# Optimization experiments

Measured on AMD Instinct MI355X. Metric: run time of the kernel, lower is better.

The kernel has to match this reference:

```python
import jax, jax.numpy as jnp
import numpy as np

EMBED_DIM = 1024
NUM_HEADS = 16
HEAD_DIM = EMBED_DIM // NUM_HEADS


def setup_inputs() -> dict:
    key = jax.random.key(0)
    kx, kw1, kb1, kw2, kb2 = jax.random.split(key, 5)
    D = EMBED_DIM
    # torch nn.Linear default init: U(-1/sqrt(in), 1/sqrt(in)); use scaled uniform
    lim = 1.0 / np.sqrt(D)
    return {
        "x": jax.random.normal(kx, (2, 2048, D), dtype=jnp.float32),
        "w_qkv": jax.random.uniform(kw1, (D, 3 * D), jnp.float32, -lim, lim),
        "b_qkv": jax.random.uniform(kb1, (3 * D,), jnp.float32, -lim, lim),
        "w_o": jax.random.uniform(kw2, (D, D), jnp.float32, -lim, lim),
        "b_o": jax.random.uniform(kb2, (D,), jnp.float32, -lim, lim),
    }


def reference(x, w_qkv, b_qkv, w_o, b_o):
    B, S, D = x.shape
    H, hd = NUM_HEADS, HEAD_DIM
    qkv = x @ w_qkv + b_qkv                       # [B,S,3D]
    qkv = qkv.reshape(B, S, H, 3, hd)             # per-head [q|k|v] blocks of size hd
    q = qkv[:, :, :, 0].transpose(0, 2, 1, 3)     # [B,H,S,hd]
    k = qkv[:, :, :, 1].transpose(0, 2, 1, 3)
    v = qkv[:, :, :, 2].transpose(0, 2, 1, 3)
    scale = hd ** -0.5
    scores = jnp.einsum('bhqd,bhkd->bhqk', q, k) * scale
    attn = jax.nn.softmax(scores, axis=-1)
    out = jnp.einsum('bhqk,bhkd->bhqd', attn, v)  # [B,H,S,hd]
    out = out.transpose(0, 2, 1, 3).reshape(B, S, D)
    return out @ w_o + b_o
```

## Files before the change

kernel.cpp:

```cpp
#include <hip/hip_runtime.h>

typedef __attribute__((ext_vector_type(8))) _Float16 half8;
typedef __attribute__((ext_vector_type(4))) _Float16 half4;
typedef __attribute__((ext_vector_type(4))) float f32x4;
typedef __attribute__((ext_vector_type(16))) float f32x16;
typedef __attribute__((ext_vector_type(4))) int i32x4;

typedef __attribute__((address_space(1))) void* gptr_t;
typedef __attribute__((address_space(3))) void* lptr_t;
#define GLL16(g, l) __builtin_amdgcn_global_load_lds((gptr_t)(g), (lptr_t)(l), 16, 0, 0)

__device__ __forceinline__ float fast_exp2(float x) {
  float r;
  asm volatile("v_exp_f32 %0, %1" : "=v"(r) : "v"(x));
  return r;
}


__global__ void prep_kernel(const float* __restrict__ x, _Float16* __restrict__ xh,
                            const float* __restrict__ w_qkv, _Float16* __restrict__ wqkvT,
                            const float* __restrict__ w_o, _Float16* __restrict__ woT) {
  __shared__ _Float16 lds[64][72];
  const int bid = blockIdx.x;
  const int t = threadIdx.x;
  if (bid < 4096) {
    size_t i = (size_t)bid * 256 + t;
    float4 v = *reinterpret_cast<const float4*>(x + i * 4);
    half4 o = { (_Float16)v.x, (_Float16)v.y, (_Float16)v.z, (_Float16)v.w };
    *reinterpret_cast<half4*>(xh + i * 4) = o;
    return;
  }
  const float* w; _Float16* wt; int N, bx, by;
  if (bid < 4096 + 768) { int b = bid - 4096; w = w_qkv; wt = wqkvT; N = 3072; bx = b % 48; by = b / 48; }
  else                  { int b = bid - 4864; w = w_o;   wt = woT;   N = 1024; bx = b & 15; by = b >> 4; }
  const int n0 = bx * 64, k0 = by * 64;
#pragma unroll
  for (int rep = 0; rep < 4; ++rep) {
    int k = rep * 16 + (t >> 4);
    int nc = (t & 15) * 4;
    float4 v = *reinterpret_cast<const float4*>(&w[(size_t)(k0 + k) * N + n0 + nc]);
    lds[nc + 0][k] = (_Float16)v.x;
    lds[nc + 1][k] = (_Float16)v.y;
    lds[nc + 2][k] = (_Float16)v.z;
    lds[nc + 3][k] = (_Float16)v.w;
  }
  __syncthreads();
#pragma unroll
  for (int rep = 0; rep < 2; ++rep) {
    int ch = rep * 256 + t;
    int n = ch >> 3, kc = ch & 7;
    half8 o = *reinterpret_cast<const half8*>(&lds[n][kc * 8]);
    *reinterpret_cast<half8*>(&wt[(size_t)(n0 + n) * 1024 + k0 + kc * 8]) = o;
  }
}


__global__ __launch_bounds__(256, 2)
void gemm_qkv(const _Float16* __restrict__ A, const _Float16* __restrict__ Bt,
              const float* __restrict__ bias,
              _Float16* __restrict__ qh, _Float16* __restrict__ kh,
              _Float16* __restrict__ vT) {
  __shared__ __align__(16) _Float16 Ah[128 * 64];
  __shared__ __align__(16) _Float16 Bh[128 * 64];
  const int t = threadIdx.x;
  const int w = t >> 6, ln = t & 63, G = ln >> 4, c = ln & 15;
  const int m0 = blockIdx.y * 128, n0 = blockIdx.x * 128;
  const int wr = w >> 1, wc = w & 1;
  f32x4 acc[4][4] = {};
  for (int kt = 0; kt < 1024; kt += 64) {
#pragma unroll
    for (int i = 0; i < 4; ++i) {
      int ch = i * 256 + t;
      int row = ch >> 3, kc = ch & 7;
      int kk = kt + ((kc ^ (row & 7)) << 3);
      int ldsbase = (i * 256 + w * 64) * 8;
      GLL16(A + (size_t)(m0 + row) * 1024 + kk, Ah + ldsbase);
      GLL16(Bt + (size_t)(n0 + row) * 1024 + kk, Bh + ldsbase);
    }
    __syncthreads();
    half8 aF[2][4], bF[2][4];
#pragma unroll
    for (int ks = 0; ks < 2; ++ks)
#pragma unroll
      for (int i = 0; i < 4; ++i) {
        int ra = wr * 64 + i * 16 + c;
        aF[ks][i] = *reinterpret_cast<const half8*>(&Ah[ra * 64 + (((ks * 4 + G) ^ (ra & 7)) << 3)]);
        int rb = wc * 64 + i * 16 + c;
        bF[ks][i] = *reinterpret_cast<const half8*>(&Bh[rb * 64 + (((ks * 4 + G) ^ (rb & 7)) << 3)]);
      }
#pragma unroll
    for (int ks = 0; ks < 2; ++ks)
#pragma unroll
      for (int mi = 0; mi < 4; ++mi)
#pragma unroll
        for (int ni = 0; ni < 4; ++ni)
          acc[mi][ni] = __builtin_amdgcn_mfma_f32_16x16x32_f16(aF[ks][mi], bF[ks][ni], acc[mi][ni], 0, 0, 0);
    __syncthreads();
  }
  const int mbase = m0 + wr * 64, nbase = n0 + wc * 64;
  const int Gp = ((G & 1) << 1) | (G >> 1);
#pragma unroll
  for (int ni = 0; ni < 4; ++ni) {
    int n = nbase + ni * 16 + c;
    float bv = bias[n];
    int h = n / 192;
    int rem = n - h * 192;
    int tt = rem >> 6, d = rem & 63;
#pragma unroll
    for (int mi = 0; mi < 4; ++mi) {
      if (tt == 2) {
        int mb = mbase + mi * 16;
        int bb = mb >> 11, s0 = mb & 2047;
        size_t bh = (size_t)(bb * 16 + h);
        half4 o = { (_Float16)(acc[mi][ni][0] + bv), (_Float16)(acc[mi][ni][1] + bv),
                    (_Float16)(acc[mi][ni][2] + bv), (_Float16)(acc[mi][ni][3] + bv) };
        *reinterpret_cast<half4*>(&vT[(bh * 64 + d) * 2048 + s0 + 4 * Gp]) = o;
      } else {
#pragma unroll
        for (int r = 0; r < 4; ++r) {
          int m = mbase + mi * 16 + 4 * G + r;
          int bb = m >> 11, s = m & 2047;
          float val = acc[mi][ni][r] + bv;
          size_t bh = (size_t)(bb * 16 + h);
          if (tt == 0) qh[(bh * 2048 + s) * 64 + d] = (_Float16)(val * (0.125f * 1.44269504089f));
          else         kh[(bh * 2048 + s) * 64 + d] = (_Float16)val;
        }
      }
    }
  }
}


__global__ __launch_bounds__(256, 2)
void gemm_o(const _Float16* __restrict__ A, const _Float16* __restrict__ Bt,
            const float* __restrict__ bias, float* __restrict__ outf) {
  __shared__ __align__(16) _Float16 Ah[128 * 64];
  __shared__ __align__(16) _Float16 Bh[64 * 64];
  const int t = threadIdx.x;
  const int w = t >> 6, ln = t & 63, G = ln >> 4, c = ln & 15;
  const int m0 = blockIdx.y * 128, n0 = blockIdx.x * 64;
  const int wr = w >> 1, wc = w & 1;
  f32x4 acc[4][2] = {};
  for (int kt = 0; kt < 1024; kt += 64) {
#pragma unroll
    for (int i = 0; i < 4; ++i) {
      int ch = i * 256 + t;
      int row = ch >> 3, kc = ch & 7;
      int kk = kt + ((kc ^ (row & 7)) << 3);
      GLL16(A + (size_t)(m0 + row) * 1024 + kk, Ah + (i * 256 + w * 64) * 8);
    }
#pragma unroll
    for (int i = 0; i < 2; ++i) {
      int ch = i * 256 + t;
      int row = ch >> 3, kc = ch & 7;
      int kk = kt + ((kc ^ (row & 7)) << 3);
      GLL16(Bt + (size_t)(n0 + row) * 1024 + kk, Bh + (i * 256 + w * 64) * 8);
    }
    __syncthreads();
    half8 aF[2][4], bF[2][2];
#pragma unroll
    for (int ks = 0; ks < 2; ++ks) {
#pragma unroll
      for (int i = 0; i < 4; ++i) {
        int ra = wr * 64 + i * 16 + c;
        aF[ks][i] = *reinterpret_cast<const half8*>(&Ah[ra * 64 + (((ks * 4 + G) ^ (ra & 7)) << 3)]);
      }
#pragma unroll
      for (int i = 0; i < 2; ++i) {
        int rb = wc * 32 + i * 16 + c;
        bF[ks][i] = *reinterpret_cast<const half8*>(&Bh[rb * 64 + (((ks * 4 + G) ^ (rb & 7)) << 3)]);
      }
    }
#pragma unroll
    for (int ks = 0; ks < 2; ++ks)
#pragma unroll
      for (int mi = 0; mi < 4; ++mi)
#pragma unroll
        for (int ni = 0; ni < 2; ++ni)
          acc[mi][ni] = __builtin_amdgcn_mfma_f32_16x16x32_f16(aF[ks][mi], bF[ks][ni], acc[mi][ni], 0, 0, 0);
    __syncthreads();
  }
  const int mbase = m0 + wr * 64, nbase = n0 + wc * 32;
#pragma unroll
  for (int ni = 0; ni < 2; ++ni) {
    int n = nbase + ni * 16 + c;
    float bv = bias[n];
#pragma unroll
    for (int mi = 0; mi < 4; ++mi)
#pragma unroll
      for (int r = 0; r < 4; ++r) {
        int m = mbase + mi * 16 + 4 * G + r;
        outf[(size_t)m * 1024 + n] = acc[mi][ni][r] + bv;
      }
  }
}


__global__ __launch_bounds__(256, 1)
void attn_kernel(const _Float16* __restrict__ qh, const _Float16* __restrict__ kh,
                 const _Float16* __restrict__ vT, _Float16* __restrict__ ao) {
  __shared__ __align__(16) _Float16 Kt[3][64 * 64];
  __shared__ __align__(16) _Float16 Vt[4][64 * 64];
  const int t = threadIdx.x;
  const int w = t >> 6, ln = t & 63, lo = ln & 31, hi = ln >> 5;
  const int bid = blockIdx.x;
  const int xcd = bid & 7, tt = bid >> 3;
  const int bh = xcd * 4 + (tt >> 4);
  const int qb = tt & 15;
  const int q0 = qb * 128 + w * 32;
  const _Float16* qp = qh + (size_t)bh * 2048 * 64;
  const _Float16* kp = kh + (size_t)bh * 2048 * 64;
  const _Float16* vp = vT + (size_t)bh * 64 * 2048;

  half8 qf[4];
#pragma unroll
  for (int sl = 0; sl < 4; ++sl)
    qf[sl] = *reinterpret_cast<const half8*>(qp + (size_t)(q0 + lo) * 64 + sl * 16 + hi * 8);

  f32x16 O0 = {}, O1 = {};
  f32x16 S0, S1;
  float plsum = 0.f;
  unsigned pk[4][4];

  auto stage = [&](int kb, int vb, int jt) {
#pragma unroll
    for (int i = 0; i < 2; ++i) {
      int ch = i * 256 + t;
      int row = ch >> 3, cc = ch & 7;
      int sw = ((cc ^ ((row ^ (row >> 3)) & 7)) << 3);
      int ldsbase = (i * 256 + w * 64) * 8;
      GLL16(kp + (size_t)(jt + row) * 64 + sw, &Kt[kb][ldsbase]);
      GLL16(vp + (size_t)row * 2048 + jt + sw, &Vt[vb][ldsbase]);
    }
  };

  auto qkt = [&](int kb) {
    f32x16 a = {}, b = {};
#pragma unroll
    for (int sl = 0; sl < 4; ++sl) {
      const int ch = sl * 2 + hi;
      const int r0 = lo, r1 = 32 + lo;
      half8 k0 = *reinterpret_cast<const half8*>(&Kt[kb][r0 * 64 + ((ch ^ ((r0 ^ (r0 >> 3)) & 7)) << 3)]);
      a = __builtin_amdgcn_mfma_f32_32x32x16_f16(k0, qf[sl], a, 0, 0, 0);
      half8 k1 = *reinterpret_cast<const half8*>(&Kt[kb][r1 * 64 + ((ch ^ ((r1 ^ (r1 >> 3)) & 7)) << 3)]);
      b = __builtin_amdgcn_mfma_f32_32x32x16_f16(k1, qf[sl], b, 0, 0, 0);
    }
    S0 = a; S1 = b;
  };

  auto pv = [&](int vb) {
#pragma unroll
    for (int kb2 = 0; kb2 < 4; ++kb2) {
      i32x4 pi = { (int)pk[kb2][0], (int)pk[kb2][1], (int)pk[kb2][2], (int)pk[kb2][3] };
      half8 pf = __builtin_bit_cast(half8, pi);
      const int ch = kb2 * 2 + hi;
      const int r0 = lo, r1 = 32 + lo;
      half8 v0 = *reinterpret_cast<const half8*>(&Vt[vb][r0 * 64 + ((ch ^ ((r0 ^ (r0 >> 3)) & 7)) << 3)]);
      O0 = __builtin_amdgcn_mfma_f32_32x32x16_f16(v0, pf, O0, 0, 0, 0);
      half8 v1 = *reinterpret_cast<const half8*>(&Vt[vb][r1 * 64 + ((ch ^ ((r1 ^ (r1 >> 3)) & 7)) << 3)]);
      O1 = __builtin_amdgcn_mfma_f32_32x32x16_f16(v1, pf, O1, 0, 0, 0);
    }
  };

  auto smpack = [&]() {
    float e0[16], e1[16];
#pragma unroll
    for (int i = 0; i < 16; ++i) e0[i] = fast_exp2(S0[i]);
#pragma unroll
    for (int i = 0; i < 16; ++i) e1[i] = fast_exp2(S1[i]);
    float sm[8];
#pragma unroll
    for (int i = 0; i < 8; ++i) sm[i] = (e0[i] + e0[i + 8]) + (e1[i] + e1[i + 8]);
#pragma unroll
    for (int i = 0; i < 4; ++i) sm[i] += sm[i + 4];
    plsum += (sm[0] + sm[1]) + (sm[2] + sm[3]);
#pragma unroll
    for (int kh2 = 0; kh2 < 2; ++kh2)
#pragma unroll
      for (int j = 0; j < 4; ++j) {
        pk[kh2][j]     = __builtin_bit_cast(unsigned, __builtin_amdgcn_cvt_pkrtz(e0[kh2 * 8 + 2 * j], e0[kh2 * 8 + 2 * j + 1]));
        pk[2 + kh2][j] = __builtin_bit_cast(unsigned, __builtin_amdgcn_cvt_pkrtz(e1[kh2 * 8 + 2 * j], e1[kh2 * 8 + 2 * j + 1]));
      }
  };

  stage(0, 0, 0);
  stage(1, 1, 64);
  stage(2, 2, 128);
  asm volatile("s_waitcnt vmcnt(8)" ::: "memory");
  __builtin_amdgcn_s_barrier();
  qkt(0);
  asm volatile("s_waitcnt vmcnt(4)" ::: "memory");
  __builtin_amdgcn_s_barrier();

  for (int it = 0; it < 31; ++it) {
    if (it < 29) {
      int T = it + 3;
      stage(T % 3, T & 3, T * 64);
    }
    smpack();
    __builtin_amdgcn_s_setprio(1);
    qkt((it + 1) % 3);
    pv(it & 3);
    __builtin_amdgcn_s_setprio(0);
    if (it < 29) asm volatile("s_waitcnt vmcnt(4)" ::: "memory");
    else         asm volatile("s_waitcnt vmcnt(0)" ::: "memory");
    __builtin_amdgcn_s_barrier();
  }
  smpack();
  pv(31 & 3);

  float lsum = plsum + __shfl_xor(plsum, 32);
  float inv = 1.f / lsum;
  const int bb = bh >> 4, hd_i = bh & 15;
  const size_t srow = (size_t)bb * 2048 + q0 + lo;
  _Float16* aob = ao + srow * 1024 + hd_i * 64 + hi * 4;
#pragma unroll
  for (int rq = 0; rq < 4; ++rq) {
    half4 o0 = { (_Float16)(O0[4 * rq] * inv), (_Float16)(O0[4 * rq + 1] * inv),
                 (_Float16)(O0[4 * rq + 2] * inv), (_Float16)(O0[4 * rq + 3] * inv) };
    *reinterpret_cast<half4*>(aob + rq * 8) = o0;
    half4 o1 = { (_Float16)(O1[4 * rq] * inv), (_Float16)(O1[4 * rq + 1] * inv),
                 (_Float16)(O1[4 * rq + 2] * inv), (_Float16)(O1[4 * rq + 3] * inv) };
    *reinterpret_cast<half4*>(aob + 32 + rq * 8) = o1;
  }
}


extern "C" void kernel_launch(void* const* d_in, const int* in_sizes, int n_in,
                              void* d_out, int out_size, void* d_ws, size_t ws_size,
                              hipStream_t stream) {
  const float* x     = (const float*)d_in[0];
  const float* w_qkv = (const float*)d_in[1];
  const float* b_qkv = (const float*)d_in[2];
  const float* w_o   = (const float*)d_in[3];
  const float* b_o   = (const float*)d_in[4];
  float* out = (float*)d_out;
  char* ws = (char*)d_ws;
  _Float16* xh    = (_Float16*)(ws);
  _Float16* wqkvT = (_Float16*)(ws + ((size_t)8  << 20));
  _Float16* woT   = (_Float16*)(ws + ((size_t)14 << 20));
  _Float16* qh    = (_Float16*)(ws + ((size_t)16 << 20));
  _Float16* kh    = (_Float16*)(ws + ((size_t)24 << 20));
  _Float16* vT    = (_Float16*)(ws + ((size_t)32 << 20));
  _Float16* ao    = (_Float16*)(ws + ((size_t)40 << 20));

  prep_kernel<<<5120, 256, 0, stream>>>(x, xh, w_qkv, wqkvT, w_o, woT);
  gemm_qkv<<<dim3(24, 32), 256, 0, stream>>>(xh, wqkvT, b_qkv, qh, kh, vT);
  attn_kernel<<<512, 256, 0, stream>>>(qh, kh, vT, ao);
  gemm_o<<<dim3(16, 32), 256, 0, stream>>>(ao, woT, b_o, out);
}
```

Measured before the change: 114.2 us.

## Double-buffer LDS tiles in QKV and output GEMMs, replace modulo with counters

Both projection GEMMs now use two LDS buffers so the global-to-LDS load of the next K tile is issued before computing on the current one, overlapping memory latency with MFMA work. The attention loop replaces the `% 3` buffer index computations with rolling counters. Doubling LDS use (64KB for QKV) may reduce occupancy below the two blocks per CU requested by the launch bounds. A single barrier per iteration relies on the hardware waiting for outstanding loads before the barrier.

```diff
diff --git a/kernel.cpp b/kernel.cpp
--- a/kernel.cpp
+++ b/kernel.cpp
@@ -60,33 +60,40 @@
               const float* __restrict__ bias,
               _Float16* __restrict__ qh, _Float16* __restrict__ kh,
               _Float16* __restrict__ vT) {
-  __shared__ __align__(16) _Float16 Ah[128 * 64];
-  __shared__ __align__(16) _Float16 Bh[128 * 64];
+  __shared__ __align__(16) _Float16 Ah[2][128 * 64];
+  __shared__ __align__(16) _Float16 Bh[2][128 * 64];
   const int t = threadIdx.x;
   const int w = t >> 6, ln = t & 63, G = ln >> 4, c = ln & 15;
   const int m0 = blockIdx.y * 128, n0 = blockIdx.x * 128;
   const int wr = w >> 1, wc = w & 1;
   f32x4 acc[4][4] = {};
-  for (int kt = 0; kt < 1024; kt += 64) {
+
+  auto stage = [&](int b, int kt) {
 #pragma unroll
     for (int i = 0; i < 4; ++i) {
       int ch = i * 256 + t;
       int row = ch >> 3, kc = ch & 7;
       int kk = kt + ((kc ^ (row & 7)) << 3);
       int ldsbase = (i * 256 + w * 64) * 8;
-      GLL16(A + (size_t)(m0 + row) * 1024 + kk, Ah + ldsbase);
-      GLL16(Bt + (size_t)(n0 + row) * 1024 + kk, Bh + ldsbase);
-    }
-    __syncthreads();
+      GLL16(A + (size_t)(m0 + row) * 1024 + kk, &Ah[b][ldsbase]);
+      GLL16(Bt + (size_t)(n0 + row) * 1024 + kk, &Bh[b][ldsbase]);
+    }
+  };
+
+  stage(0, 0);
+  __syncthreads();
+  int buf = 0;
+  for (int kt = 0; kt < 1024; kt += 64) {
+    if (kt < 960) stage(buf ^ 1, kt + 64);
     half8 aF[2][4], bF[2][4];
 #pragma unroll
     for (int ks = 0; ks < 2; ++ks)
 #pragma unroll
       for (int i = 0; i < 4; ++i) {
         int ra = wr * 64 + i * 16 + c;
-        aF[ks][i] = *reinterpret_cast<const half8*>(&Ah[ra * 64 + (((ks * 4 + G) ^ (ra & 7)) << 3)]);
+        aF[ks][i] = *reinterpret_cast<const half8*>(&Ah[buf][ra * 64 + (((ks * 4 + G) ^ (ra & 7)) << 3)]);
         int rb = wc * 64 + i * 16 + c;
-        bF[ks][i] = *reinterpret_cast<const half8*>(&Bh[rb * 64 + (((ks * 4 + G) ^ (rb & 7)) << 3)]);
+        bF[ks][i] = *reinterpret_cast<const half8*>(&Bh[buf][rb * 64 + (((ks * 4 + G) ^ (rb & 7)) << 3)]);
       }
 #pragma unroll
     for (int ks = 0; ks < 2; ++ks)
@@ -96,6 +103,7 @@
         for (int ni = 0; ni < 4; ++ni)
           acc[mi][ni] = __builtin_amdgcn_mfma_f32_16x16x32_f16(aF[ks][mi], bF[ks][ni], acc[mi][ni], 0, 0, 0);
     __syncthreads();
+    buf ^= 1;
   }
   const int mbase = m0 + wr * 64, nbase = n0 + wc * 64;
   const int Gp = ((G & 1) << 1) | (G >> 1);
@@ -134,41 +142,48 @@
 __global__ __launch_bounds__(256, 2)
 void gemm_o(const _Float16* __restrict__ A, const _Float16* __restrict__ Bt,
             const float* __restrict__ bias, float* __restrict__ outf) {
-  __shared__ __align__(16) _Float16 Ah[128 * 64];
-  __shared__ __align__(16) _Float16 Bh[64 * 64];
+  __shared__ __align__(16) _Float16 Ah[2][128 * 64];
+  __shared__ __align__(16) _Float16 Bh[2][64 * 64];
   const int t = threadIdx.x;
   const int w = t >> 6, ln = t & 63, G = ln >> 4, c = ln & 15;
   const int m0 = blockIdx.y * 128, n0 = blockIdx.x * 64;
   const int wr = w >> 1, wc = w & 1;
   f32x4 acc[4][2] = {};
-  for (int kt = 0; kt < 1024; kt += 64) {
+
+  auto stage = [&](int b, int kt) {
 #pragma unroll
     for (int i = 0; i < 4; ++i) {
       int ch = i * 256 + t;
       int row = ch >> 3, kc = ch & 7;
       int kk = kt + ((kc ^ (row & 7)) << 3);
-      GLL16(A + (size_t)(m0 + row) * 1024 + kk, Ah + (i * 256 + w * 64) * 8);
+      GLL16(A + (size_t)(m0 + row) * 1024 + kk, &Ah[b][(i * 256 + w * 64) * 8]);
     }
 #pragma unroll
     for (int i = 0; i < 2; ++i) {
       int ch = i * 256 + t;
       int row = ch >> 3, kc = ch & 7;
       int kk = kt + ((kc ^ (row & 7)) << 3);
-      GLL16(Bt + (size_t)(n0 + row) * 1024 + kk, Bh + (i * 256 + w * 64) * 8);
-    }
-    __syncthreads();
+      GLL16(Bt + (size_t)(n0 + row) * 1024 + kk, &Bh[b][(i * 256 + w * 64) * 8]);
+    }
+  };
+
+  stage(0, 0);
+  __syncthreads();
+  int buf = 0;
+  for (int kt = 0; kt < 1024; kt += 64) {
+    if (kt < 960) stage(buf ^ 1, kt + 64);
     half8 aF[2][4], bF[2][2];
 #pragma unroll
     for (int ks = 0; ks < 2; ++ks) {
 #pragma unroll
       for (int i = 0; i < 4; ++i) {
         int ra = wr * 64 + i * 16 + c;
-        aF[ks][i] = *reinterpret_cast<const half8*>(&Ah[ra * 64 + (((ks * 4 + G) ^ (ra & 7)) << 3)]);
+        aF[ks][i] = *reinterpret_cast<const half8*>(&Ah[buf][ra * 64 + (((ks * 4 + G) ^ (ra & 7)) << 3)]);
       }
 #pragma unroll
       for (int i = 0; i < 2; ++i) {
         int rb = wc * 32 + i * 16 + c;
-        bF[ks][i] = *reinterpret_cast<const half8*>(&Bh[rb * 64 + (((ks * 4 + G) ^ (rb & 7)) << 3)]);
+        bF[ks][i] = *reinterpret_cast<const half8*>(&Bh[buf][rb * 64 + (((ks * 4 + G) ^ (rb & 7)) << 3)]);
       }
     }
 #pragma unroll
@@ -179,6 +194,7 @@
         for (int ni = 0; ni < 2; ++ni)
           acc[mi][ni] = __builtin_amdgcn_mfma_f32_16x16x32_f16(aF[ks][mi], bF[ks][ni], acc[mi][ni], 0, 0, 0);
     __syncthreads();
+    buf ^= 1;
   }
   const int mbase = m0 + wr * 64, nbase = n0 + wc * 32;
 #pragma unroll
@@ -292,19 +308,19 @@
   asm volatile("s_waitcnt vmcnt(4)" ::: "memory");
   __builtin_amdgcn_s_barrier();
 
+  int kb_w = 0, kb_n = 1;
   for (int it = 0; it < 31; ++it) {
-    if (it < 29) {
-      int T = it + 3;
-      stage(T % 3, T & 3, T * 64);
-    }
+    if (it < 29) stage(kb_w, (it + 3) & 3, (it + 3) * 64);
     smpack();
     __builtin_amdgcn_s_setprio(1);
-    qkt((it + 1) % 3);
+    qkt(kb_n);
     pv(it & 3);
     __builtin_amdgcn_s_setprio(0);
     if (it < 29) asm volatile("s_waitcnt vmcnt(4)" ::: "memory");
     else         asm volatile("s_waitcnt vmcnt(0)" ::: "memory");
     __builtin_amdgcn_s_barrier();
+    if (++kb_w == 3) kb_w = 0;
+    if (++kb_n == 3) kb_n = 0;
   }
   smpack();
   pv(31 & 3);
```

Result: no change. 116.0 us (+1.6%).

## Widen attention KV tile to 128 keys with double-buffered K and triple-buffered V

Applied to the files above, without the earlier changes.

The attention kernel now processes 128 keys per iteration instead of 64. K uses two LDS buffers and V three, with a 16-chunk XOR swizzle for the wider V rows. The main loop is unrolled by two and waits for all outstanding loads (vmcnt(0)) before each barrier. This halves the number of loop iterations and barriers, at the cost of more registers for S and P and a shallower prefetch pipeline, which could expose load latency.

```diff
diff --git a/kernel.cpp b/kernel.cpp
--- a/kernel.cpp
+++ b/kernel.cpp
@@ -199,8 +199,8 @@
 __global__ __launch_bounds__(256, 1)
 void attn_kernel(const _Float16* __restrict__ qh, const _Float16* __restrict__ kh,
                  const _Float16* __restrict__ vT, _Float16* __restrict__ ao) {
-  __shared__ __align__(16) _Float16 Kt[3][64 * 64];
-  __shared__ __align__(16) _Float16 Vt[4][64 * 64];
+  __shared__ __align__(16) _Float16 Kt[2][128 * 64];
+  __shared__ __align__(16) _Float16 Vt[3][64 * 128];
   const int t = threadIdx.x;
   const int w = t >> 6, ln = t & 63, lo = ln & 31, hi = ln >> 5;
   const int bid = blockIdx.x;
@@ -218,96 +218,118 @@
     qf[sl] = *reinterpret_cast<const half8*>(qp + (size_t)(q0 + lo) * 64 + sl * 16 + hi * 8);
 
   f32x16 O0 = {}, O1 = {};
-  f32x16 S0, S1;
+  f32x16 S0, S1, S2, S3;
   float plsum = 0.f;
-  unsigned pk[4][4];
-
-  auto stage = [&](int kb, int vb, int jt) {
-#pragma unroll
-    for (int i = 0; i < 2; ++i) {
+  unsigned pk[8][4];
+
+  auto stageK = [&](int kb, int jt) {
+#pragma unroll
+    for (int i = 0; i < 4; ++i) {
       int ch = i * 256 + t;
       int row = ch >> 3, cc = ch & 7;
-      int sw = ((cc ^ ((row ^ (row >> 3)) & 7)) << 3);
-      int ldsbase = (i * 256 + w * 64) * 8;
-      GLL16(kp + (size_t)(jt + row) * 64 + sw, &Kt[kb][ldsbase]);
-      GLL16(vp + (size_t)row * 2048 + jt + sw, &Vt[vb][ldsbase]);
+      int sw = (cc ^ ((row ^ (row >> 3)) & 7)) << 3;
+      GLL16(kp + (size_t)(jt + row) * 64 + sw, &Kt[kb][(i * 256 + w * 64) * 8]);
+    }
+  };
+  auto stageV = [&](int vb, int jt) {
+#pragma unroll
+    for (int i = 0; i < 4; ++i) {
+      int ch = i * 256 + t;
+      int row = ch >> 4, cc = ch & 15;
+      int sw = (cc ^ ((row ^ (row >> 4)) & 15)) << 3;
+      GLL16(vp + (size_t)row * 2048 + jt + sw, &Vt[vb][(i * 256 + w * 64) * 8]);
     }
   };
 
   auto qkt = [&](int kb) {
-    f32x16 a = {}, b = {};
+    f32x16 a0 = {}, a1 = {}, a2 = {}, a3 = {};
 #pragma unroll
     for (int sl = 0; sl < 4; ++sl) {
       const int ch = sl * 2 + hi;
-      const int r0 = lo, r1 = 32 + lo;
+      const int r0 = lo, r1 = 32 + lo, r2 = 64 + lo, r3 = 96 + lo;
       half8 k0 = *reinterpret_cast<const half8*>(&Kt[kb][r0 * 64 + ((ch ^ ((r0 ^ (r0 >> 3)) & 7)) << 3)]);
-      a = __builtin_amdgcn_mfma_f32_32x32x16_f16(k0, qf[sl], a, 0, 0, 0);
+      a0 = __builtin_amdgcn_mfma_f32_32x32x16_f16(k0, qf[sl], a0, 0, 0, 0);
       half8 k1 = *reinterpret_cast<const half8*>(&Kt[kb][r1 * 64 + ((ch ^ ((r1 ^ (r1 >> 3)) & 7)) << 3)]);
-      b = __builtin_amdgcn_mfma_f32_32x32x16_f16(k1, qf[sl], b, 0, 0, 0);
-    }
-    S0 = a; S1 = b;
+      a1 = __builtin_amdgcn_mfma_f32_32x32x16_f16(k1, qf[sl], a1, 0, 0, 0);
+      half8 k2 = *reinterpret_cast<const half8*>(&Kt[kb][r2 * 64 + ((ch ^ ((r2 ^ (r2 >> 3)) & 7)) << 3)]);
+      a2 = __builtin_amdgcn_mfma_f32_32x32x16_f16(k2, qf[sl], a2, 0, 0, 0);
+      half8 k3 = *reinterpret_cast<const half8*>(&Kt[kb][r3 * 64 + ((ch ^ ((r3 ^ (r3 >> 3)) & 7)) << 3)]);
+      a3 = __builtin_amdgcn_mfma_f32_32x32x16_f16(k3, qf[sl], a3, 0, 0, 0);
+    }
+    S0 = a0; S1 = a1; S2 = a2; S3 = a3;
   };
 
   auto pv = [&](int vb) {
 #pragma unroll
-    for (int kb2 = 0; kb2 < 4; ++kb2) {
+    for (int kb2 = 0; kb2 < 8; ++kb2) {
       i32x4 pi = { (int)pk[kb2][0], (int)pk[kb2][1], (int)pk[kb2][2], (int)pk[kb2][3] };
       half8 pf = __builtin_bit_cast(half8, pi);
       const int ch = kb2 * 2 + hi;
       const int r0 = lo, r1 = 32 + lo;
-      half8 v0 = *reinterpret_cast<const half8*>(&Vt[vb][r0 * 64 + ((ch ^ ((r0 ^ (r0 >> 3)) & 7)) << 3)]);
+      half8 v0 = *reinterpret_cast<const half8*>(&Vt[vb][r0 * 128 + ((ch ^ ((r0 ^ (r0 >> 4)) & 15)) << 3)]);
       O0 = __builtin_amdgcn_mfma_f32_32x32x16_f16(v0, pf, O0, 0, 0, 0);
-      half8 v1 = *reinterpret_cast<const half8*>(&Vt[vb][r1 * 64 + ((ch ^ ((r1 ^ (r1 >> 3)) & 7)) << 3)]);
+      half8 v1 = *reinterpret_cast<const half8*>(&Vt[vb][r1 * 128 + ((ch ^ ((r1 ^ (r1 >> 4)) & 15)) << 3)]);
       O1 = __builtin_amdgcn_mfma_f32_32x32x16_f16(v1, pf, O1, 0, 0, 0);
     }
   };
 
-  auto smpack = [&]() {
-    float e0[16], e1[16];
-#pragma unroll
-    for (int i = 0; i < 16; ++i) e0[i] = fast_exp2(S0[i]);
-#pragma unroll
-    for (int i = 0; i < 16; ++i) e1[i] = fast_exp2(S1[i]);
-    float sm[8];
-#pragma unroll
-    for (int i = 0; i < 8; ++i) sm[i] = (e0[i] + e0[i + 8]) + (e1[i] + e1[i + 8]);
-#pragma unroll
-    for (int i = 0; i < 4; ++i) sm[i] += sm[i + 4];
-    plsum += (sm[0] + sm[1]) + (sm[2] + sm[3]);
+  auto smp1 = [&](f32x16& S, int base) {
+    float e[16];
+#pragma unroll
+    for (int i = 0; i < 16; ++i) e[i] = fast_exp2(S[i]);
+    float s4[4];
+#pragma unroll
+    for (int i = 0; i < 4; ++i) s4[i] = (e[i] + e[i + 4]) + (e[i + 8] + e[i + 12]);
+    plsum += (s4[0] + s4[1]) + (s4[2] + s4[3]);
 #pragma unroll
     for (int kh2 = 0; kh2 < 2; ++kh2)
 #pragma unroll
-      for (int j = 0; j < 4; ++j) {
-        pk[kh2][j]     = __builtin_bit_cast(unsigned, __builtin_amdgcn_cvt_pkrtz(e0[kh2 * 8 + 2 * j], e0[kh2 * 8 + 2 * j + 1]));
-        pk[2 + kh2][j] = __builtin_bit_cast(unsigned, __builtin_amdgcn_cvt_pkrtz(e1[kh2 * 8 + 2 * j], e1[kh2 * 8 + 2 * j + 1]));
-      }
-  };
-
-  stage(0, 0, 0);
-  stage(1, 1, 64);
-  stage(2, 2, 128);
+      for (int j = 0; j < 4; ++j)
+        pk[base + kh2][j] = __builtin_bit_cast(unsigned,
+            __builtin_amdgcn_cvt_pkrtz(e[kh2 * 8 + 2 * j], e[kh2 * 8 + 2 * j + 1]));
+  };
+  auto smpack = [&]() { smp1(S0, 0); smp1(S1, 2); smp1(S2, 4); smp1(S3, 6); };
+
+  stageK(0, 0);   stageV(0, 0);
+  stageK(1, 128); stageV(1, 128);
   asm volatile("s_waitcnt vmcnt(8)" ::: "memory");
   __builtin_amdgcn_s_barrier();
   qkt(0);
-  asm volatile("s_waitcnt vmcnt(4)" ::: "memory");
+  asm volatile("s_waitcnt vmcnt(0)" ::: "memory");
   __builtin_amdgcn_s_barrier();
 
-  for (int it = 0; it < 31; ++it) {
-    if (it < 29) {
-      int T = it + 3;
-      stage(T % 3, T & 3, T * 64);
-    }
+  int vbr = 0, vbw = 2;
+  auto bump3 = [](int& v) { if (++v == 3) v = 0; };
+#pragma unroll 1
+  for (int it2 = 0; it2 < 7; ++it2) {
+    const int tE = 2 * it2;
+    stageK(0, (tE + 2) * 128); stageV(vbw, (tE + 2) * 128);
     smpack();
     __builtin_amdgcn_s_setprio(1);
-    qkt((it + 1) % 3);
-    pv(it & 3);
+    qkt(1);
+    pv(vbr);
     __builtin_amdgcn_s_setprio(0);
-    if (it < 29) asm volatile("s_waitcnt vmcnt(4)" ::: "memory");
-    else         asm volatile("s_waitcnt vmcnt(0)" ::: "memory");
+    asm volatile("s_waitcnt vmcnt(0)" ::: "memory");
     __builtin_amdgcn_s_barrier();
+    bump3(vbr); bump3(vbw);
+    stageK(1, (tE + 3) * 128); stageV(vbw, (tE + 3) * 128);
+    smpack();
+    __builtin_amdgcn_s_setprio(1);
+    qkt(0);
+    pv(vbr);
+    __builtin_amdgcn_s_setprio(0);
+    asm volatile("s_waitcnt vmcnt(0)" ::: "memory");
+    __builtin_amdgcn_s_barrier();
+    bump3(vbr); bump3(vbw);
   }
   smpack();
-  pv(31 & 3);
+  __builtin_amdgcn_s_setprio(1);
+  qkt(1);
+  pv(vbr);
+  __builtin_amdgcn_s_setprio(0);
+  bump3(vbr);
+  smpack();
+  pv(vbr);
 
   float lsum = plsum + __shfl_xor(plsum, 32);
   float inv = 1.f / lsum;
```

Result: slower. 119.2 us (+4.4%).
